# Kernel optimization log

Measured on AMD Instinct MI355X. Metric: run time of the kernel, lower is better.

Reference implementation:

```python
import jax, jax.numpy as jnp
import numpy as np
import math

D_MODEL = 2048
N_HEAD = 16
D_HEAD = D_MODEL // N_HEAD
B, T = 4, 2048


def bitlinear(x, w):
    # gamma: global abs-mean scale of the weight, clamped
    gamma = jnp.maximum(jnp.mean(jnp.abs(w)), 1e-5)
    w_quant = jnp.clip(jnp.round(w / gamma), -1.0, 1.0)
    # straight-through estimator: forward uses ternary weights, grad flows to w
    w_eff = jax.lax.stop_gradient(w_quant - w) + w
    return jnp.matmul(x, w_eff.T) * gamma


def setup_inputs() -> dict:
    key = jax.random.key(0)
    kx, kq, kk, kv, ko = jax.random.split(key, 5)
    s = 0.02
    return {
        "x": jax.random.normal(kx, (B, T, D_MODEL), dtype=jnp.float32),
        "wq": jax.random.normal(kq, (D_MODEL, D_MODEL), dtype=jnp.float32) * s,
        "wk": jax.random.normal(kk, (D_MODEL, D_MODEL), dtype=jnp.float32) * s,
        "wv": jax.random.normal(kv, (D_MODEL, D_MODEL), dtype=jnp.float32) * s,
        "wo": jax.random.normal(ko, (D_MODEL, D_MODEL), dtype=jnp.float32) * s,
    }


def reference(x, wq, wk, wv, wo):
    b, t, c = x.shape
    # BitLinear QKV projections -> (B, H, T, Dh)
    def split_heads(y):
        return y.reshape(b, t, N_HEAD, D_HEAD).transpose(0, 2, 1, 3)

    q = split_heads(bitlinear(x, wq))
    k = split_heads(bitlinear(x, wk))
    v = split_heads(bitlinear(x, wv))

    scale = 1.0 / math.sqrt(D_HEAD)
    scores = jnp.einsum("bhqd,bhkd->bhqk", q, k) * scale  # (B,H,T,T)
    causal = jnp.tril(jnp.ones((t, t), dtype=bool))
    scores = jnp.where(causal, scores, jnp.finfo(scores.dtype).min)
    attn = jax.nn.softmax(scores, axis=-1)
    out = jnp.einsum("bhqk,bhkd->bhqd", attn, v)  # (B,H,T,Dh)
    out = out.transpose(0, 2, 1, 3).reshape(b, t, c)
    return bitlinear(out, wo)
```

## Files before the change

kernel.cpp:

```cpp
#include <hip/hip_runtime.h>
#include <stdint.h>

#define D_MODEL 2048
#define NHEAD   16
#define DHEAD   128
#define BATCH   4
#define SEQ     2048
#define MROWS   (BATCH*SEQ)
#define WELEMS  (D_MODEL*D_MODEL)
#define NITEMS  2048

typedef __attribute__((ext_vector_type(4))) float          f32x4;
typedef __attribute__((ext_vector_type(8))) short          s16x8;
typedef __attribute__((ext_vector_type(4))) unsigned short u16x4;

__device__ __forceinline__ unsigned short f2bf(float f) {
  union { float f; uint32_t u; } v; v.f = f;
  uint32_t r = v.u + 0x7fffu + ((v.u >> 16) & 1u);
  return (unsigned short)(r >> 16);
}

__device__ __forceinline__ void load_lds16(const void* g, void* l) {
  __builtin_amdgcn_global_load_lds(
      (__attribute__((address_space(1))) void*)(g),
      (__attribute__((address_space(3))) void*)(l), 16, 0, 0);
}

__device__ __forceinline__ float gamma_of(const double* sums, int gidx) {
  double gs = sums[gidx] * (1.0 / (double)WELEMS);
  if (gs < 1e-5) gs = 1e-5;
  return (float)gs;
}

__global__ __launch_bounds__(256) void absmean_kernel(
    const float* __restrict__ w0, const float* __restrict__ w1,
    const float* __restrict__ w2, const float* __restrict__ w3,
    double* __restrict__ sums) {
  const float* w = blockIdx.y == 0 ? w0 : blockIdx.y == 1 ? w1
                 : blockIdx.y == 2 ? w2 : w3;
  double acc = 0.0;
  const int stride = gridDim.x * blockDim.x;
  for (int i = blockIdx.x * blockDim.x + threadIdx.x; i < WELEMS / 4; i += stride) {
    float4 v = ((const float4*)w)[i];
    acc += (double)fabsf(v.x) + (double)fabsf(v.y) +
           (double)fabsf(v.z) + (double)fabsf(v.w);
  }
  acc += __shfl_xor(acc, 1);  acc += __shfl_xor(acc, 2);  acc += __shfl_xor(acc, 4);
  acc += __shfl_xor(acc, 8);  acc += __shfl_xor(acc, 16); acc += __shfl_xor(acc, 32);
  __shared__ double wsum[4];
  const int lane = threadIdx.x & 63, wave = threadIdx.x >> 6;
  if (lane == 0) wsum[wave] = acc;
  __syncthreads();
  if (threadIdx.x == 0)
    atomicAdd(&sums[blockIdx.y], wsum[0] + wsum[1] + wsum[2] + wsum[3]);
}

__global__ __launch_bounds__(256) void quant_kernel(
    const float* __restrict__ wsrc, unsigned short* __restrict__ wt,
    const double* __restrict__ sums, int gidx) {
  const float gf = gamma_of(sums, gidx);
  const int i = blockIdx.x * 256 + threadIdx.x;
  float4 v = ((const float4*)wsrc)[i];
  u16x4 r;
  r[0] = f2bf(fminf(1.f, fmaxf(-1.f, rintf(v.x / gf))));
  r[1] = f2bf(fminf(1.f, fmaxf(-1.f, rintf(v.y / gf))));
  r[2] = f2bf(fminf(1.f, fmaxf(-1.f, rintf(v.z / gf))));
  r[3] = f2bf(fminf(1.f, fmaxf(-1.f, rintf(v.w / gf))));
  ((u16x4*)wt)[i] = r;
}

__global__ __launch_bounds__(256) void cvt_bf16_kernel(
    const float* __restrict__ x, unsigned short* __restrict__ xb) {
  const int i = blockIdx.x * 256 + threadIdx.x;
  float4 v = ((const float4*)x)[i];
  u16x4 r;
  r[0] = f2bf(v.x); r[1] = f2bf(v.y); r[2] = f2bf(v.z); r[3] = f2bf(v.w);
  ((u16x4*)xb)[i] = r;
}

template <int MODE>
__global__ __launch_bounds__(256) void gemm_bt_kernel(
    const unsigned short* __restrict__ A,
    const unsigned short* __restrict__ Bt,
    void* __restrict__ out,
    const double* __restrict__ sums, int gidx, float escale) {
  constexpr int K = D_MODEL;
  __shared__ unsigned short As[128 * 32];
  __shared__ unsigned short Bs[128 * 32];
  const int tid = threadIdx.x, lane = tid & 63, wave = tid >> 6;
  const int g = lane >> 4, r15 = lane & 15;
  const int wm = wave >> 1, wn = wave & 1;

  const int lin = blockIdx.y * 16 + blockIdx.x;
  const int wg  = (lin & 7) * 128 + (lin >> 3);
  const int rowBase = (wg >> 4) * 128, colBase = (wg & 15) * 128;

  f32x4 acc[4][4] = {};

  const int o0 = wave * 1024 + lane * 16;
  const int o1 = 4096 + wave * 1024 + lane * 16;
  const unsigned short* Ap0 = A  + (size_t)(rowBase + (o0 >> 6)) * K + ((o0 >> 4) & 3) * 8;
  const unsigned short* Ap1 = A  + (size_t)(rowBase + (o1 >> 6)) * K + ((o1 >> 4) & 3) * 8;
  const unsigned short* Bp0 = Bt + (size_t)(colBase + (o0 >> 6)) * K + ((o0 >> 4) & 3) * 8;
  const unsigned short* Bp1 = Bt + (size_t)(colBase + (o1 >> 6)) * K + ((o1 >> 4) & 3) * 8;
  char* AsB = (char*)As; char* BsB = (char*)Bs;

  for (int kt = 0; kt < K; kt += 32) {
    load_lds16(Ap0 + kt, AsB + wave * 1024);
    load_lds16(Ap1 + kt, AsB + 4096 + wave * 1024);
    load_lds16(Bp0 + kt, BsB + wave * 1024);
    load_lds16(Bp1 + kt, BsB + 4096 + wave * 1024);
    __syncthreads();
    s16x8 a[4], b[4];
#pragma unroll
    for (int m = 0; m < 4; ++m)
      a[m] = *(const s16x8*)(AsB + (wm * 64 + m * 16 + r15) * 64 + g * 16);
#pragma unroll
    for (int n = 0; n < 4; ++n)
      b[n] = *(const s16x8*)(BsB + (wn * 64 + n * 16 + r15) * 64 + g * 16);
#pragma unroll
    for (int m = 0; m < 4; ++m)
#pragma unroll
      for (int n = 0; n < 4; ++n)
        acc[m][n] = __builtin_amdgcn_mfma_f32_16x16x32_bf16(a[m], b[n], acc[m][n], 0, 0, 0);
    __syncthreads();
  }

  const float scale = gamma_of(sums, gidx) * escale;
#pragma unroll
  for (int m = 0; m < 4; ++m) {
    const int row0 = rowBase + wm * 64 + m * 16 + g * 4;
#pragma unroll
    for (int n = 0; n < 4; ++n) {
      const int col = colBase + wn * 64 + n * 16 + r15;
      if constexpr (MODE == 2) {
        float* op = (float*)out;
#pragma unroll
        for (int j = 0; j < 4; ++j)
          op[(size_t)(row0 + j) * D_MODEL + col] = acc[m][n][j] * scale;
      } else if constexpr (MODE == 0) {
        unsigned short* op = (unsigned short*)out;
#pragma unroll
        for (int j = 0; j < 4; ++j)
          op[(size_t)(row0 + j) * D_MODEL + col] = f2bf(acc[m][n][j] * scale);
      } else {
        unsigned short* op = (unsigned short*)out;
        const int bb = row0 >> 11, t = row0 & 2047;
        const int hh = col >> 7,  d = col & 127;
        u16x4 r;
#pragma unroll
        for (int j = 0; j < 4; ++j) r[j] = f2bf(acc[m][n][j] * scale);
        *(u16x4*)(op + (((size_t)bb * NHEAD + hh) * DHEAD + d) * SEQ + t) = r;
      }
    }
  }
}

__global__ __launch_bounds__(256, 4) void attn_kernel(
    const unsigned short* __restrict__ qg,
    const unsigned short* __restrict__ kg,
    const unsigned short* __restrict__ vtg,
    unsigned short* __restrict__ og,
    int* __restrict__ counter) {
  __shared__ unsigned short Ks[64 * 128];
  __shared__ unsigned short Vts[128 * 64];
  __shared__ unsigned short Ps[4][1024];
  __shared__ int s_item;

  const int tid = threadIdx.x, lane = tid & 63, wave = tid >> 6;
  const int g = lane >> 4, r15 = lane & 15;

  char* KsB = (char*)Ks; char* VtsB = (char*)Vts; char* PsB = (char*)(Ps[wave]);

  for (;;) {
    if (tid == 0) s_item = atomicAdd(counter, 1);
    __syncthreads();
    const int item = s_item;
    __syncthreads();
    if (item >= NITEMS) break;

    const int qs = 31 - (item >> 6);
    const int bh = item & 63;
    const int b = bh >> 4, h = bh & 15;

    const unsigned short* kbase = kg + (size_t)b * SEQ * D_MODEL + h * DHEAD;
    const unsigned short* vbase = vtg + (size_t)(b * NHEAD + h) * DHEAD * SEQ;

    s16x8 qf[4];
    {
      const unsigned short* qbase =
          qg + (size_t)(b * SEQ + qs * 64 + wave * 16 + r15) * D_MODEL + h * DHEAD;
#pragma unroll
      for (int c = 0; c < 4; ++c) qf[c] = *(const s16x8*)(qbase + c * 32 + g * 8);
    }

    f32x4 oacc[8] = {};
    float mr[4], lr[4];
#pragma unroll
    for (int j = 0; j < 4; ++j) { mr[j] = -1e30f; lr[j] = 0.f; }

    const int nt = qs + 1;

#pragma unroll 1
    for (int t = 0; t < nt; ++t) {
#pragma unroll
      for (int rnd = 0; rnd < 4; ++rnd) {
        const int ob = rnd * 4096 + wave * 1024 + lane * 16;
        const int krow = ob >> 8;
        const int ks = (ob & 255) ^ ((krow & 7) << 4);
        load_lds16(kbase + (size_t)(t * 64 + krow) * D_MODEL + (ks >> 1),
                   KsB + rnd * 4096 + wave * 1024);
        const int drow = ob >> 7;
        const int vs = (ob & 127) ^ ((drow & 7) << 4);
        load_lds16(vbase + (size_t)drow * SEQ + t * 64 + (vs >> 1),
                   VtsB + rnd * 4096 + wave * 1024);
      }
      __syncthreads();

      f32x4 s[4] = {};
      __builtin_amdgcn_s_setprio(1);
#pragma unroll
      for (int c = 0; c < 4; ++c) {
#pragma unroll
        for (int n = 0; n < 4; ++n) {
          const int key = n * 16 + r15;
          const int baddr = (((key << 8) | (c << 6) | (g << 4))) ^ ((key & 7) << 4);
          s16x8 kf = *(const s16x8*)(KsB + baddr);
          s[n] = __builtin_amdgcn_mfma_f32_16x16x32_bf16(qf[c], kf, s[n], 0, 0, 0);
        }
      }
      __builtin_amdgcn_s_setprio(0);

      if (t == qs) {
        const int q0 = qs * 64 + wave * 16 + g * 4;
        const int k0 = t * 64 + r15;
#pragma unroll
        for (int n = 0; n < 4; ++n)
#pragma unroll
          for (int j = 0; j < 4; ++j)
            if (k0 + n * 16 > q0 + j) s[n][j] = -1e30f;
      }
      float pm[4];
#pragma unroll
      for (int j = 0; j < 4; ++j)
        pm[j] = fmaxf(fmaxf(s[0][j], s[1][j]), fmaxf(s[2][j], s[3][j]));
#pragma unroll
      for (int j = 0; j < 4; ++j) {
        pm[j] = fmaxf(pm[j], __shfl_xor(pm[j], 1));
        pm[j] = fmaxf(pm[j], __shfl_xor(pm[j], 2));
        pm[j] = fmaxf(pm[j], __shfl_xor(pm[j], 4));
        pm[j] = fmaxf(pm[j], __shfl_xor(pm[j], 8));
      }
      bool ok = pm[0] <= mr[0] + 8.f && pm[1] <= mr[1] + 8.f &&
                pm[2] <= mr[2] + 8.f && pm[3] <= mr[3] + 8.f;
      if (!__all(ok)) {
#pragma unroll
        for (int j = 0; j < 4; ++j) {
          const float mn = fmaxf(mr[j], pm[j]);
          const float rf = exp2f(mr[j] - mn);
          mr[j] = mn;
          lr[j] *= rf;
#pragma unroll
          for (int n2 = 0; n2 < 8; ++n2) oacc[n2][j] *= rf;
        }
      }
      float psum[4] = {0.f, 0.f, 0.f, 0.f};
#pragma unroll
      for (int n = 0; n < 4; ++n) {
        const int keyl = n * 16 + r15;
#pragma unroll
        for (int j = 0; j < 4; ++j) {
          const float p = exp2f(s[n][j] - mr[j]);
          psum[j] += p;
          const int row = g * 4 + j;
          const int baddr = ((row << 7) | (keyl << 1)) ^ ((row & 7) << 4);
          *(unsigned short*)(PsB + baddr) = f2bf(p);
        }
      }
#pragma unroll
      for (int j = 0; j < 4; ++j) {
        psum[j] += __shfl_xor(psum[j], 1);
        psum[j] += __shfl_xor(psum[j], 2);
        psum[j] += __shfl_xor(psum[j], 4);
        psum[j] += __shfl_xor(psum[j], 8);
        lr[j] += psum[j];
      }
      __builtin_amdgcn_s_setprio(1);
#pragma unroll
      for (int c2 = 0; c2 < 2; ++c2) {
        const int baddr_p = (((r15 << 7) | (c2 << 6) | (g << 4))) ^ ((r15 & 7) << 4);
        s16x8 pa = *(const s16x8*)(PsB + baddr_p);
#pragma unroll
        for (int n2 = 0; n2 < 8; ++n2) {
          const int d = n2 * 16 + r15;
          const int baddr_v = (((d << 7) | (c2 << 6) | (g << 4))) ^ ((d & 7) << 4);
          s16x8 vf = *(const s16x8*)(VtsB + baddr_v);
          oacc[n2] = __builtin_amdgcn_mfma_f32_16x16x32_bf16(pa, vf, oacc[n2], 0, 0, 0);
        }
      }
      __builtin_amdgcn_s_setprio(0);
      __syncthreads();
    }

    unsigned short* obase =
        og + (size_t)(b * SEQ + qs * 64 + wave * 16 + g * 4) * D_MODEL + h * DHEAD;
    float inv[4];
#pragma unroll
    for (int j = 0; j < 4; ++j) inv[j] = 1.f / lr[j];
#pragma unroll
    for (int n2 = 0; n2 < 8; ++n2) {
      const int d = n2 * 16 + r15;
#pragma unroll
      for (int j = 0; j < 4; ++j)
        obase[(size_t)j * D_MODEL + d] = f2bf(oacc[n2][j] * inv[j]);
    }
  }
}

extern "C" void kernel_launch(void* const* d_in, const int* in_sizes, int n_in,
                              void* d_out, int out_size, void* d_ws, size_t ws_size,
                              hipStream_t stream) {
  const float* x  = (const float*)d_in[0];
  const float* wq = (const float*)d_in[1];
  const float* wk = (const float*)d_in[2];
  const float* wv = (const float*)d_in[3];
  const float* wo = (const float*)d_in[4];
  float* out = (float*)d_out;

  char* ws = (char*)d_ws;
  double* sums = (double*)ws;
  int* cnt = (int*)(ws + 64);
  size_t off = 256;
  unsigned short* wtern = (unsigned short*)(ws + off); off += (size_t)WELEMS * 2;
  unsigned short* xbf   = (unsigned short*)(ws + off); off += (size_t)MROWS * D_MODEL * 2;
  unsigned short* qb    = (unsigned short*)(ws + off); off += (size_t)MROWS * D_MODEL * 2;
  unsigned short* kb    = (unsigned short*)(ws + off); off += (size_t)MROWS * D_MODEL * 2;
  unsigned short* vtb   = (unsigned short*)(ws + off); off += (size_t)MROWS * D_MODEL * 2;
  unsigned short* attn_out = xbf;

  hipMemsetAsync(ws, 0, 256, stream);
  absmean_kernel<<<dim3(256, 4), 256, 0, stream>>>(wq, wk, wv, wo, sums);
  cvt_bf16_kernel<<<MROWS * D_MODEL / 4 / 256, 256, 0, stream>>>(x, xbf);

  const float qfold = 0.08838834764831845f * 1.4426950408889634f;

  const dim3 ggrid(D_MODEL / 128, MROWS / 128);
  quant_kernel<<<WELEMS / 4 / 256, 256, 0, stream>>>(wq, wtern, sums, 0);
  gemm_bt_kernel<0><<<ggrid, 256, 0, stream>>>(xbf, wtern, qb, sums, 0, qfold);
  quant_kernel<<<WELEMS / 4 / 256, 256, 0, stream>>>(wk, wtern, sums, 1);
  gemm_bt_kernel<0><<<ggrid, 256, 0, stream>>>(xbf, wtern, kb, sums, 1, 1.0f);
  quant_kernel<<<WELEMS / 4 / 256, 256, 0, stream>>>(wv, wtern, sums, 2);
  gemm_bt_kernel<1><<<ggrid, 256, 0, stream>>>(xbf, wtern, vtb, sums, 2, 1.0f);

  attn_kernel<<<dim3(1024), 256, 0, stream>>>(qb, kb, vtb, attn_out, cnt);

  quant_kernel<<<WELEMS / 4 / 256, 256, 0, stream>>>(wo, wtern, sums, 3);
  gemm_bt_kernel<2><<<ggrid, 256, 0, stream>>>(attn_out, wtern, out, sums, 3, 1.0f);
}
```

Before: 741.4 us.

## Use 256x256 GEMM tiles with triple-buffered LDS prefetch and swizzle

Rewrites the BitLinear projection GEMM to use 256x256 output tiles per 512-thread block, with a three-stage LDS ring buffer filled by direct global-to-LDS loads two k-steps ahead. It also adds an XOR swizzle on LDS rows, splits the MFMA work into two halves interleaved with prefetch issue, and raises wave priority around MFMA bursts. The intent is to hide global load latency and raise data reuse per tile. In exchange it needs 96KB of dynamic shared memory and runs a grid of 256 blocks with one block per CU.

```diff
diff --git a/kernel.cpp b/kernel.cpp
--- a/kernel.cpp
+++ b/kernel.cpp
@@ -79,78 +79,120 @@
 }
 
 template <int MODE>
-__global__ __launch_bounds__(256) void gemm_bt_kernel(
+__global__ __launch_bounds__(512, 2) void gemm_bt_kernel(
     const unsigned short* __restrict__ A,
     const unsigned short* __restrict__ Bt,
     void* __restrict__ out,
     const double* __restrict__ sums, int gidx, float escale) {
   constexpr int K = D_MODEL;
-  __shared__ unsigned short As[128 * 32];
-  __shared__ unsigned short Bs[128 * 32];
+  constexpr int NT = K / 32;
+  extern __shared__ char smem[];
+
   const int tid = threadIdx.x, lane = tid & 63, wave = tid >> 6;
   const int g = lane >> 4, r15 = lane & 15;
-  const int wm = wave >> 1, wn = wave & 1;
-
-  const int lin = blockIdx.y * 16 + blockIdx.x;
-  const int wg  = (lin & 7) * 128 + (lin >> 3);
-  const int rowBase = (wg >> 4) * 128, colBase = (wg & 15) * 128;
-
-  f32x4 acc[4][4] = {};
-
-  const int o0 = wave * 1024 + lane * 16;
-  const int o1 = 4096 + wave * 1024 + lane * 16;
-  const unsigned short* Ap0 = A  + (size_t)(rowBase + (o0 >> 6)) * K + ((o0 >> 4) & 3) * 8;
-  const unsigned short* Ap1 = A  + (size_t)(rowBase + (o1 >> 6)) * K + ((o1 >> 4) & 3) * 8;
-  const unsigned short* Bp0 = Bt + (size_t)(colBase + (o0 >> 6)) * K + ((o0 >> 4) & 3) * 8;
-  const unsigned short* Bp1 = Bt + (size_t)(colBase + (o1 >> 6)) * K + ((o1 >> 4) & 3) * 8;
-  char* AsB = (char*)As; char* BsB = (char*)Bs;
-
-  for (int kt = 0; kt < K; kt += 32) {
-    load_lds16(Ap0 + kt, AsB + wave * 1024);
-    load_lds16(Ap1 + kt, AsB + 4096 + wave * 1024);
-    load_lds16(Bp0 + kt, BsB + wave * 1024);
-    load_lds16(Bp1 + kt, BsB + 4096 + wave * 1024);
-    __syncthreads();
-    s16x8 a[4], b[4];
-#pragma unroll
-    for (int m = 0; m < 4; ++m)
-      a[m] = *(const s16x8*)(AsB + (wm * 64 + m * 16 + r15) * 64 + g * 16);
-#pragma unroll
-    for (int n = 0; n < 4; ++n)
-      b[n] = *(const s16x8*)(BsB + (wn * 64 + n * 16 + r15) * 64 + g * 16);
-#pragma unroll
-    for (int m = 0; m < 4; ++m)
-#pragma unroll
-      for (int n = 0; n < 4; ++n)
-        acc[m][n] = __builtin_amdgcn_mfma_f32_16x16x32_bf16(a[m], b[n], acc[m][n], 0, 0, 0);
-    __syncthreads();
+  const int wm = wave >> 2, wn = wave & 3;
+
+  const int wgid = (blockIdx.x & 7) * 32 + (blockIdx.x >> 3);
+  const int rowBase = (wgid >> 3) * 256, colBase = (wgid & 7) * 256;
+
+  const int o0 = tid * 16, o1 = 8192 + tid * 16;
+  const int sr0 = o0 >> 6, sc0 = (o0 & 63) ^ ((sr0 & 3) << 4);
+  const int sr1 = o1 >> 6, sc1 = (o1 & 63) ^ ((sr1 & 3) << 4);
+  const unsigned short* ApS0 = A  + (size_t)(rowBase + sr0) * K + (sc0 >> 1);
+  const unsigned short* ApS1 = A  + (size_t)(rowBase + sr1) * K + (sc1 >> 1);
+  const unsigned short* BpS0 = Bt + (size_t)(colBase + sr0) * K + (sc0 >> 1);
+  const unsigned short* BpS1 = Bt + (size_t)(colBase + sr1) * K + (sc1 >> 1);
+
+  char* b0 = smem; char* b1 = smem + 32768; char* b2 = smem + 65536;
+  const int woff = wave * 1024;
+
+  const int sw = (g * 16) ^ ((r15 & 3) << 4);
+  const int arow = wm * 128 + r15;
+  const int brow = wn * 64 + r15;
+
+  f32x4 acc[8][4] = {};
+
+  load_lds16(ApS0, b0 + woff);          load_lds16(ApS1, b0 + 8192 + woff);
+  load_lds16(BpS0, b0 + 16384 + woff);  load_lds16(BpS1, b0 + 24576 + woff);
+  load_lds16(ApS0 + 32, b1 + woff);         load_lds16(ApS1 + 32, b1 + 8192 + woff);
+  load_lds16(BpS0 + 32, b1 + 16384 + woff); load_lds16(BpS1 + 32, b1 + 24576 + woff);
+  asm volatile("s_waitcnt vmcnt(4)" ::: "memory");
+  __builtin_amdgcn_sched_barrier(0);
+  __builtin_amdgcn_s_barrier();
+  __builtin_amdgcn_sched_barrier(0);
+
+#pragma unroll 1
+  for (int t = 0; t < NT; ++t) {
+    const bool pf = (t + 2 < NT);
+    const int koff = (t + 2) * 32;
+
+    if (pf) {
+      load_lds16(ApS0 + koff, b2 + woff);
+      load_lds16(ApS1 + koff, b2 + 8192 + woff);
+    }
+    s16x8 bf[4], af[4];
+#pragma unroll
+    for (int fn = 0; fn < 4; ++fn)
+      bf[fn] = *(const s16x8*)(b0 + 16384 + (brow + fn * 16) * 64 + sw);
+#pragma unroll
+    for (int fr = 0; fr < 4; ++fr)
+      af[fr] = *(const s16x8*)(b0 + (arow + fr * 16) * 64 + sw);
+    __builtin_amdgcn_s_setprio(1);
+#pragma unroll
+    for (int fr = 0; fr < 4; ++fr)
+#pragma unroll
+      for (int fn = 0; fn < 4; ++fn)
+        acc[fr][fn] = __builtin_amdgcn_mfma_f32_16x16x32_bf16(af[fr], bf[fn], acc[fr][fn], 0, 0, 0);
+    __builtin_amdgcn_s_setprio(0);
+
+    if (pf) {
+      load_lds16(BpS0 + koff, b2 + 16384 + woff);
+      load_lds16(BpS1 + koff, b2 + 24576 + woff);
+    }
+#pragma unroll
+    for (int fr = 0; fr < 4; ++fr)
+      af[fr] = *(const s16x8*)(b0 + (arow + (fr + 4) * 16) * 64 + sw);
+    __builtin_amdgcn_s_setprio(1);
+#pragma unroll
+    for (int fr = 0; fr < 4; ++fr)
+#pragma unroll
+      for (int fn = 0; fn < 4; ++fn)
+        acc[fr + 4][fn] = __builtin_amdgcn_mfma_f32_16x16x32_bf16(af[fr], bf[fn], acc[fr + 4][fn], 0, 0, 0);
+    __builtin_amdgcn_s_setprio(0);
+
+    if (pf) asm volatile("s_waitcnt vmcnt(4)" ::: "memory");
+    else    asm volatile("s_waitcnt vmcnt(0)" ::: "memory");
+    __builtin_amdgcn_sched_barrier(0);
+    __builtin_amdgcn_s_barrier();
+    __builtin_amdgcn_sched_barrier(0);
+    char* tmp = b0; b0 = b1; b1 = b2; b2 = tmp;
   }
 
   const float scale = gamma_of(sums, gidx) * escale;
 #pragma unroll
-  for (int m = 0; m < 4; ++m) {
-    const int row0 = rowBase + wm * 64 + m * 16 + g * 4;
-#pragma unroll
-    for (int n = 0; n < 4; ++n) {
-      const int col = colBase + wn * 64 + n * 16 + r15;
+  for (int fr = 0; fr < 8; ++fr) {
+    const int row0 = rowBase + wm * 128 + fr * 16 + g * 4;
+#pragma unroll
+    for (int fn = 0; fn < 4; ++fn) {
+      const int col = colBase + wn * 64 + fn * 16 + r15;
       if constexpr (MODE == 2) {
         float* op = (float*)out;
 #pragma unroll
         for (int j = 0; j < 4; ++j)
-          op[(size_t)(row0 + j) * D_MODEL + col] = acc[m][n][j] * scale;
+          op[(size_t)(row0 + j) * D_MODEL + col] = acc[fr][fn][j] * scale;
       } else if constexpr (MODE == 0) {
         unsigned short* op = (unsigned short*)out;
 #pragma unroll
         for (int j = 0; j < 4; ++j)
-          op[(size_t)(row0 + j) * D_MODEL + col] = f2bf(acc[m][n][j] * scale);
+          op[(size_t)(row0 + j) * D_MODEL + col] = f2bf(acc[fr][fn][j] * scale);
       } else {
         unsigned short* op = (unsigned short*)out;
-        const int bb = row0 >> 11, t = row0 & 2047;
+        const int bb = row0 >> 11, tt = row0 & 2047;
         const int hh = col >> 7,  d = col & 127;
         u16x4 r;
 #pragma unroll
-        for (int j = 0; j < 4; ++j) r[j] = f2bf(acc[m][n][j] * scale);
-        *(u16x4*)(op + (((size_t)bb * NHEAD + hh) * DHEAD + d) * SEQ + t) = r;
+        for (int j = 0; j < 4; ++j) r[j] = f2bf(acc[fr][fn][j] * scale);
+        *(u16x4*)(op + (((size_t)bb * NHEAD + hh) * DHEAD + d) * SEQ + tt) = r;
       }
     }
   }
@@ -344,16 +386,17 @@
 
   const float qfold = 0.08838834764831845f * 1.4426950408889634f;
 
-  const dim3 ggrid(D_MODEL / 128, MROWS / 128);
+  const int ggrid = (MROWS / 256) * (D_MODEL / 256);
+  const int glds = 98304;
   quant_kernel<<<WELEMS / 4 / 256, 256, 0, stream>>>(wq, wtern, sums, 0);
-  gemm_bt_kernel<0><<<ggrid, 256, 0, stream>>>(xbf, wtern, qb, sums, 0, qfold);
+  gemm_bt_kernel<0><<<ggrid, 512, glds, stream>>>(xbf, wtern, qb, sums, 0, qfold);
   quant_kernel<<<WELEMS / 4 / 256, 256, 0, stream>>>(wk, wtern, sums, 1);
-  gemm_bt_kernel<0><<<ggrid, 256, 0, stream>>>(xbf, wtern, kb, sums, 1, 1.0f);
+  gemm_bt_kernel<0><<<ggrid, 512, glds, stream>>>(xbf, wtern, kb, sums, 1, 1.0f);
   quant_kernel<<<WELEMS / 4 / 256, 256, 0, stream>>>(wv, wtern, sums, 2);
-  gemm_bt_kernel<1><<<ggrid, 256, 0, stream>>>(xbf, wtern, vtb, sums, 2, 1.0f);
+  gemm_bt_kernel<1><<<ggrid, 512, glds, stream>>>(xbf, wtern, vtb, sums, 2, 1.0f);
 
   attn_kernel<<<dim3(1024), 256, 0, stream>>>(qb, kb, vtb, attn_out, cnt);
 
   quant_kernel<<<WELEMS / 4 / 256, 256, 0, stream>>>(wo, wtern, sums, 3);
-  gemm_bt_kernel<2><<<ggrid, 256, 0, stream>>>(attn_out, wtern, out, sums, 3, 1.0f);
-}
+  gemm_bt_kernel<2><<<ggrid, 512, glds, stream>>>(attn_out, wtern, out, sums, 3, 1.0f);
+}
```

Result: faster. 633.8 us (-14.5%).
